# Kernel optimization log

Hardware: AMD Instinct MI355X
Metric: run time of the kernel (lower is better)

Reference implementation:

```python
import jax, jax.numpy as jnp
import numpy as np

NEG_INF = -1e30

def _rotate_half(x):
    x1, x2 = jnp.split(x, 2, axis=-1)
    return jnp.concatenate([-x2, x1], axis=-1)

def _apply_rope(x, sin, cos):
    # x: [b, t, h, d]; sin/cos: [t, d]
    s = sin[None, :, None, :]
    c = cos[None, :, None, :]
    return x * c + _rotate_half(x) * s

def setup_inputs() -> dict:
    key = jax.random.key(0)
    ks = jax.random.split(key, 5)
    B, T, D, H = 2, 2048, 2048, 16
    hd = D // H
    x = jax.random.normal(ks[0], (B, T, D), dtype=jnp.float32)
    sin = jax.random.normal(ks[1], (T, hd), dtype=jnp.float32)
    cos = jax.random.normal(ks[2], (T, hd), dtype=jnp.float32)
    W_qkv = jax.random.normal(ks[3], (D, D + 2 * hd), dtype=jnp.float32) * (1.0 / np.sqrt(D))
    W_o = jax.random.normal(ks[4], (D, D), dtype=jnp.float32) * (1.0 / np.sqrt(D))
    return {"x": x, "sin": sin, "cos": cos, "W_qkv": W_qkv, "W_o": W_o}

def reference(x, sin, cos, W_qkv, W_o):
    B, T, D = x.shape
    num_heads = 16
    head_dim = D // num_heads
    scale = head_dim ** (-0.5)

    qkv = x @ W_qkv                              # [B, T, D + 2*hd]
    q, k, v = jnp.split(qkv, [D, D + head_dim], axis=-1)
    # q -> [B, H, T, hd]; k, v single KV head -> [B, 1, T, hd]
    q = q.reshape(B, T, num_heads, head_dim).transpose(0, 2, 1, 3)
    k = k[:, :, None, :].transpose(0, 2, 1, 3)   # [B, 1, T, hd]
    v = v[:, :, None, :].transpose(0, 2, 1, 3)

    # module scales q by head_dim^-0.5 BEFORE rope/attention
    q = q * scale

    # apply_rope_safe: transpose to [B, T, H, hd], apply rope, transpose back
    q = _apply_rope(q.transpose(0, 2, 1, 3), sin, cos).transpose(0, 2, 1, 3)
    k = _apply_rope(k.transpose(0, 2, 1, 3), sin, cos).transpose(0, 2, 1, 3)

    k0 = k[:, 0]                                 # [B, T, hd] (MQA shared KV)
    v0 = v[:, 0]

    # jax.nn.dot_product_attention applies its own 1/sqrt(hd) scaling on top
    scores = jnp.einsum('bhqd,bkd->bhqk', q, k0) * scale
    causal = jnp.tril(jnp.ones((T, T), dtype=bool))
    scores = jnp.where(causal[None, None], scores, NEG_INF)
    probs = jax.nn.softmax(scores, axis=-1)
    out = jnp.einsum('bhqk,bkd->bhqd', probs, v0)  # [B, H, T, hd]

    out = out.transpose(0, 2, 1, 3).reshape(B, T, D)
    return out @ W_o
```

## Files before the change

### kernel.cpp

```cpp
#include <hip/hip_runtime.h>
#include <stdint.h>

typedef __bf16 bf16x8_t __attribute__((ext_vector_type(8)));
typedef float f32x4_t __attribute__((ext_vector_type(4)));

#define AS1 __attribute__((address_space(1)))
#define AS3 __attribute__((address_space(3)))

static __device__ __forceinline__ unsigned short f2bf(float f) {
  union { float f; unsigned u; } a;
  a.f = f;
  unsigned r = a.u + 0x7fffu + ((a.u >> 16) & 1u);
  return (unsigned short)(r >> 16);
}

static __device__ __forceinline__ unsigned pack2bf(float lo, float hi) {
  return (unsigned)f2bf(lo) | ((unsigned)f2bf(hi) << 16);
}

__global__ void cvt_bf16_kernel(const float* __restrict__ in, unsigned short* __restrict__ out) {
  long i = ((long)blockIdx.x * blockDim.x + threadIdx.x) * 4;
  float4 v = *(const float4*)(in + i);
  ushort4 o;
  o.x = f2bf(v.x);
  o.y = f2bf(v.y);
  o.z = f2bf(v.z);
  o.w = f2bf(v.w);
  *(ushort4*)(out + i) = o;
}

__global__ void transpose_f32_bf16(const float* __restrict__ src, unsigned short* __restrict__ dst,
                                   int ld, int dld, long sbs, long dbs) {
  __shared__ float tile[64][65];
  src += (long)blockIdx.z * sbs;
  dst += (long)blockIdx.z * dbs;
  const int c0 = blockIdx.x * 64, r0 = blockIdx.y * 64;
  const int tx = threadIdx.x, ty = threadIdx.y;
#pragma unroll
  for (int j = 0; j < 64; j += 4)
    tile[ty + j][tx] = src[(long)(r0 + ty + j) * ld + (c0 + tx)];
  __syncthreads();
#pragma unroll
  for (int j = 0; j < 64; j += 4)
    dst[(long)(c0 + ty + j) * dld + (r0 + tx)] = f2bf(tile[tx][ty + j]);
}

__global__ __launch_bounds__(256) void gemm_bt(const unsigned short* __restrict__ A,
                                               const unsigned short* __restrict__ Bt,
                                               float* __restrict__ C,
                                               int M, int N, int K) {
  __shared__ unsigned short As[128 * 32];
  __shared__ unsigned short Bs[128 * 32];
  const int tid = threadIdx.x;
  const int wid = tid >> 6, lane = tid & 63;
  const int r16 = lane & 15, g = lane >> 4;
  const long bm = (long)blockIdx.y * 128;
  const long bn = (long)blockIdx.x * 128;
  const int wr = (wid >> 1) * 64, wc = (wid & 1) * 64;
  f32x4_t acc[4][4];
#pragma unroll
  for (int i = 0; i < 4; i++)
#pragma unroll
    for (int j = 0; j < 4; j++) acc[i][j] = (f32x4_t){0.f, 0.f, 0.f, 0.f};

  for (int kt = 0; kt < K; kt += 32) {
#pragma unroll
    for (int i = 0; i < 2; i++) {
      const int chunk = (i * 4 + wid) * 64 + lane;
      const int row = chunk >> 2, col = (chunk & 3) * 8;
      __builtin_amdgcn_global_load_lds(
          (const AS1 void*)(A + (bm + row) * K + kt + col),
          (AS3 void*)(As + chunk * 8), 16, 0, 0);
      __builtin_amdgcn_global_load_lds(
          (const AS1 void*)(Bt + (bn + row) * K + kt + col),
          (AS3 void*)(Bs + chunk * 8), 16, 0, 0);
    }
    __syncthreads();
    bf16x8_t af[4], bfr[4];
#pragma unroll
    for (int mi = 0; mi < 4; mi++)
      af[mi] = *(const bf16x8_t*)(As + (wr + mi * 16 + r16) * 32 + g * 8);
#pragma unroll
    for (int ni = 0; ni < 4; ni++)
      bfr[ni] = *(const bf16x8_t*)(Bs + (wc + ni * 16 + r16) * 32 + g * 8);
#pragma unroll
    for (int mi = 0; mi < 4; mi++)
#pragma unroll
      for (int ni = 0; ni < 4; ni++)
        acc[mi][ni] = __builtin_amdgcn_mfma_f32_16x16x32_bf16(af[mi], bfr[ni], acc[mi][ni], 0, 0, 0);
    __syncthreads();
  }
#pragma unroll
  for (int mi = 0; mi < 4; mi++)
#pragma unroll
    for (int ni = 0; ni < 4; ni++) {
      const long rowb = bm + wr + mi * 16 + 4 * g;
      const long colb = bn + wc + ni * 16 + r16;
#pragma unroll
      for (int j = 0; j < 4; j++)
        C[(rowb + j) * N + colb] = acc[mi][ni][j];
    }
}

__global__ void rope_kernel(const float* __restrict__ qkv,
                            const float* __restrict__ sinp,
                            const float* __restrict__ cosp,
                            unsigned short* __restrict__ qr,
                            unsigned short* __restrict__ kr) {
  const int row = blockIdx.x;
  const int b = row >> 11, t = row & 2047;
  const float* src = qkv + (long)row * 2304;
  const int tid = threadIdx.x;
  const int d = tid & 127;
  const int dp = (d + 64) & 127;
  const float c = cosp[t * 128 + d];
  const float s = sinp[t * 128 + d];
  const float sgn = (d < 64) ? -1.f : 1.f;
  for (int h = (tid >> 7); h < 16; h += 2) {
    const float x0 = src[h * 128 + d];
    const float xp = src[h * 128 + dp];
    qr[((long)((b * 16 + h) * 2048 + t)) * 128 + d] = f2bf((x0 * c + sgn * xp * s) * 0.0078125f);
  }
  if (tid < 128) {
    const float x0 = src[2048 + d];
    const float xp = src[2048 + dp];
    kr[((long)(b * 2048 + t)) * 128 + d] = f2bf(x0 * c + sgn * xp * s);
  }
}

__global__ __launch_bounds__(256, 2)
void mqa_attn(const unsigned short* __restrict__ qr,
              const unsigned short* __restrict__ kr,
              const unsigned short* __restrict__ vT,
              unsigned short* __restrict__ ao) {
  __shared__ unsigned short Kb[2][64 * 128];
  __shared__ unsigned short Vb[128 * 64];
  __shared__ unsigned short plds[4][16 * 64];
  const int idx = blockIdx.x;
  const int pj = idx & 15, h = (idx >> 4) & 15, b = idx >> 8;
  const int tid = threadIdx.x;
  const int wid = tid >> 6, lane = tid & 63;
  const int r = lane & 15, g = lane >> 4;
  const int rs = r & 7;
  char* pw = (char*)&plds[wid][0];

  const unsigned short* kbase = kr + (long)b * 2048 * 128;
  const unsigned short* vbase = vT + (long)b * 128 * 2048;
  const unsigned short* qh = qr + (long)(b * 16 + h) * 2048 * 128;

  const int scol = (tid & 15) ^ ((tid >> 4) & 7);
  const int vscol = (tid & 7) ^ ((tid >> 3) & 7);

  f32x4_t o[8];
#pragma unroll
  for (int i = 0; i < 8; i++) o[i] = (f32x4_t){0.f, 0.f, 0.f, 0.f};
  float m = 0.f, lsum = 0.f;

  int tile = pj;
  bf16x8_t qf[4];
  {
    const unsigned short* qp = qh + (long)(tile * 64 + wid * 16 + r) * 128 + g * 8;
#pragma unroll
    for (int c = 0; c < 4; c++) qf[c] = *(const bf16x8_t*)(qp + c * 32);
  }

#pragma unroll
  for (int i = 0; i < 4; i++) {
    const int row = i * 16 + (tid >> 4);
    __builtin_amdgcn_global_load_lds(
        (const AS1 void*)(kbase + (long)row * 128 + scol * 8),
        (AS3 void*)(&Kb[0][(i * 256 + tid) * 8]), 16, 0, 0);
  }
  asm volatile("s_waitcnt vmcnt(0)" ::: "memory");
  __builtin_amdgcn_s_barrier();

  const int switch_s = pj + 1;
  for (int s = 0; s <= 32; s++) {
    const int cur = s & 1;
    const int kv0 = (s <= pj) ? 64 * s : 64 * (s - 1 - pj);

    if (s == switch_s) {
      float lt = lsum;
      lt += __shfl_xor(lt, 16);
      lt += __shfl_xor(lt, 32);
      float rl[4];
#pragma unroll
      for (int jj = 0; jj < 4; jj++) rl[jj] = 1.0f / __shfl(lt, 4 * g + jj);
      unsigned short* aop = ao + ((long)(b * 2048 + tile * 64 + wid * 16 + 4 * g)) * 2048 + h * 128 + r;
#pragma unroll
      for (int dt = 0; dt < 8; dt++)
#pragma unroll
        for (int jj = 0; jj < 4; jj++)
          aop[(long)jj * 2048 + dt * 16] = f2bf(o[dt][jj] * rl[jj]);
      tile = 31 - pj;
      const unsigned short* qp = qh + (long)(tile * 64 + wid * 16 + r) * 128 + g * 8;
#pragma unroll
      for (int c = 0; c < 4; c++) qf[c] = *(const bf16x8_t*)(qp + c * 32);
#pragma unroll
      for (int i = 0; i < 8; i++) o[i] = (f32x4_t){0.f, 0.f, 0.f, 0.f};
      m = 0.f;
      lsum = 0.f;
    }

#pragma unroll
    for (int i = 0; i < 4; i++) {
      const int vrow = i * 32 + (tid >> 3);
      __builtin_amdgcn_global_load_lds(
          (const AS1 void*)(vbase + (long)vrow * 2048 + kv0 + vscol * 8),
          (AS3 void*)(&Vb[(i * 256 + tid) * 8]), 16, 0, 0);
    }
    if (s < 32) {
      const int kvn = (s + 1 <= pj) ? 64 * (s + 1) : 64 * (s - pj);
#pragma unroll
      for (int i = 0; i < 4; i++) {
        const int row = i * 16 + (tid >> 4);
        __builtin_amdgcn_global_load_lds(
            (const AS1 void*)(kbase + (long)(kvn + row) * 128 + scol * 8),
            (AS3 void*)(&Kb[cur ^ 1][(i * 256 + tid) * 8]), 16, 0, 0);
      }
    }
    __builtin_amdgcn_sched_barrier(0);

    f32x4_t sc[4];
#pragma unroll
    for (int t = 0; t < 4; t++) sc[t] = (f32x4_t){0.f, 0.f, 0.f, 0.f};
    const unsigned short* Kcur = &Kb[cur][0];
    __builtin_amdgcn_s_setprio(1);
#pragma unroll
    for (int t = 0; t < 4; t++) {
      const unsigned short* krow = Kcur + (16 * t + r) * 128;
#pragma unroll
      for (int c = 0; c < 4; c++) {
        const bf16x8_t kf = *(const bf16x8_t*)(krow + (((4 * c + g) ^ rs) << 3));
        sc[t] = __builtin_amdgcn_mfma_f32_16x16x32_bf16(kf, qf[c], sc[t], 0, 0, 0);
      }
    }
    __builtin_amdgcn_s_setprio(0);

    if (s == pj || s == 32) {
#pragma unroll
      for (int t = 0; t < 4; t++)
#pragma unroll
        for (int jj = 0; jj < 4; jj++)
          if (t * 16 + 4 * g + jj > wid * 16 + r) sc[t][jj] = -1e30f;
    }
    float lm = sc[0][0];
#pragma unroll
    for (int t = 0; t < 4; t++)
#pragma unroll
      for (int jj = 0; jj < 4; jj++) lm = fmaxf(lm, sc[t][jj]);
    if (!__all(lm <= m + 8.f)) {
      float pm = lm;
      pm = fmaxf(pm, __shfl_xor(pm, 16));
      pm = fmaxf(pm, __shfl_xor(pm, 32));
      const float mnew = fmaxf(m, pm);
      const float alpha = __expf(m - mnew);
      lsum *= alpha;
      float aj[4];
#pragma unroll
      for (int jj = 0; jj < 4; jj++) aj[jj] = __shfl(alpha, 4 * g + jj);
#pragma unroll
      for (int dt = 0; dt < 8; dt++) {
        o[dt][0] *= aj[0]; o[dt][1] *= aj[1]; o[dt][2] *= aj[2]; o[dt][3] *= aj[3];
      }
      m = mnew;
    }
    float p[16];
#pragma unroll
    for (int t = 0; t < 4; t++)
#pragma unroll
      for (int jj = 0; jj < 4; jj++) p[4 * t + jj] = __expf(sc[t][jj] - m);
    float ls = 0.f;
#pragma unroll
    for (int i = 0; i < 16; i++) ls += p[i];
    lsum += ls;

    asm volatile("" ::: "memory");
#pragma unroll
    for (int t = 0; t < 4; t++) {
      uint2 w = {pack2bf(p[4 * t], p[4 * t + 1]), pack2bf(p[4 * t + 2], p[4 * t + 3])};
      *(uint2*)(pw + r * 128 + (((2 * t + (g >> 1)) ^ rs) << 4) + ((g & 1) << 3)) = w;
    }
    asm volatile("s_waitcnt lgkmcnt(0)" ::: "memory");
    const bf16x8_t pa0 = *(const bf16x8_t*)(pw + r * 128 + ((g ^ rs) << 4));
    const bf16x8_t pa1 = *(const bf16x8_t*)(pw + r * 128 + (((4 + g) ^ rs) << 4));

    if (s < 32)
      asm volatile("s_waitcnt vmcnt(4)" ::: "memory");
    else
      asm volatile("s_waitcnt vmcnt(0)" ::: "memory");
    __builtin_amdgcn_s_barrier();

    __builtin_amdgcn_s_setprio(1);
#pragma unroll
    for (int dt = 0; dt < 8; dt++) {
      const bf16x8_t vfA = *(const bf16x8_t*)(Vb + (dt * 16 + r) * 64 + ((g ^ rs) << 3));
      o[dt] = __builtin_amdgcn_mfma_f32_16x16x32_bf16(pa0, vfA, o[dt], 0, 0, 0);
    }
#pragma unroll
    for (int dt = 0; dt < 8; dt++) {
      const bf16x8_t vfB = *(const bf16x8_t*)(Vb + (dt * 16 + r) * 64 + (((4 + g) ^ rs) << 3));
      o[dt] = __builtin_amdgcn_mfma_f32_16x16x32_bf16(pa1, vfB, o[dt], 0, 0, 0);
    }
    __builtin_amdgcn_s_setprio(0);

    asm volatile("s_waitcnt vmcnt(0)" ::: "memory");
    __builtin_amdgcn_s_barrier();
  }
  {
    float lt = lsum;
    lt += __shfl_xor(lt, 16);
    lt += __shfl_xor(lt, 32);
    float rl[4];
#pragma unroll
    for (int jj = 0; jj < 4; jj++) rl[jj] = 1.0f / __shfl(lt, 4 * g + jj);
    unsigned short* aop = ao + ((long)(b * 2048 + tile * 64 + wid * 16 + 4 * g)) * 2048 + h * 128 + r;
#pragma unroll
    for (int dt = 0; dt < 8; dt++)
#pragma unroll
      for (int jj = 0; jj < 4; jj++)
        aop[(long)jj * 2048 + dt * 16] = f2bf(o[dt][jj] * rl[jj]);
  }
}

extern "C" void kernel_launch(void* const* d_in, const int* in_sizes, int n_in,
                              void* d_out, int out_size, void* d_ws, size_t ws_size,
                              hipStream_t stream) {
  const float* x    = (const float*)d_in[0];
  const float* sinp = (const float*)d_in[1];
  const float* cosp = (const float*)d_in[2];
  const float* Wqkv = (const float*)d_in[3];
  const float* Wo   = (const float*)d_in[4];
  float* out = (float*)d_out;
  char* ws = (char*)d_ws;

  const int B = 2, T = 2048, D = 2048, H = 16, HD = 128;
  const int M = B * T;
  const int NQ = D + 2 * HD;

  unsigned short* xb    = (unsigned short*)(ws + 0);
  unsigned short* wqkvT = (unsigned short*)(ws + 16777216);
  unsigned short* woT   = (unsigned short*)(ws + 26214400);
  float*          qkv   = (float*)         (ws + 34603008);
  unsigned short* qr    = (unsigned short*)(ws + 72351744);
  unsigned short* kr    = (unsigned short*)(ws + 89128960);
  unsigned short* vT    = (unsigned short*)(ws + 90177536);
  unsigned short* ao    = xb;

  dim3 tb(64, 4);
  cvt_bf16_kernel<<<(M * D) / 1024, 256, 0, stream>>>(x, xb);
  transpose_f32_bf16<<<dim3(NQ / 64, D / 64, 1), tb, 0, stream>>>(Wqkv, wqkvT, NQ, D, 0, 0);
  transpose_f32_bf16<<<dim3(D / 64, D / 64, 1), tb, 0, stream>>>(Wo, woT, D, D, 0, 0);
  gemm_bt<<<dim3(NQ / 128, M / 128), 256, 0, stream>>>(xb, wqkvT, qkv, M, NQ, D);
  rope_kernel<<<M, 256, 0, stream>>>(qkv, sinp, cosp, qr, kr);
  transpose_f32_bf16<<<dim3(HD / 64, T / 64, B), tb, 0, stream>>>(
      qkv + 2176, vT, NQ, T, (long)T * NQ, (long)HD * T);
  mqa_attn<<<dim3(512), 256, 0, stream>>>(qr, kr, vT, ao);
  gemm_bt<<<dim3(D / 128, M / 128), 256, 0, stream>>>(ao, woT, out, M, D, D);
}
```

Measured before the change: 223.3 us.

## Split-K both GEMMs in two with atomic accumulation and XCD-aware block swizzle

Both projection GEMMs now split the K dimension in half, launching twice as many workgroups that each accumulate partial results into zero-initialized outputs with float atomicAdd. A block-index swizzle maps consecutive blocks across the eight XCDs for better L2 locality. This targets low occupancy of the 128x128-tile grid (about 288 and 256 tiles on 256 CUs). It adds two zeroing kernels, atomic write traffic and extra memory passes over the fp32 outputs.

After: 296.5 us. 1.33x slower.

```diff
diff --git a/kernel.cpp b/kernel.cpp
--- a/kernel.cpp
+++ b/kernel.cpp
@@ -16,6 +16,11 @@
 
 static __device__ __forceinline__ unsigned pack2bf(float lo, float hi) {
   return (unsigned)f2bf(lo) | ((unsigned)f2bf(hi) << 16);
+}
+
+__global__ void zero_f32(float* __restrict__ p, long n4) {
+  long i = (long)blockIdx.x * blockDim.x + threadIdx.x;
+  if (i < n4) *(float4*)(p + i * 4) = make_float4(0.f, 0.f, 0.f, 0.f);
 }
 
 __global__ void cvt_bf16_kernel(const float* __restrict__ in, unsigned short* __restrict__ out) {
@@ -45,17 +50,28 @@
     dst[(long)(c0 + ty + j) * dld + (r0 + tx)] = f2bf(tile[tx][ty + j]);
 }
 
-__global__ __launch_bounds__(256) void gemm_bt(const unsigned short* __restrict__ A,
-                                               const unsigned short* __restrict__ Bt,
-                                               float* __restrict__ C,
-                                               int M, int N, int K) {
+__global__ __launch_bounds__(256) void gemm_bt_sk(const unsigned short* __restrict__ A,
+                                                  const unsigned short* __restrict__ Bt,
+                                                  float* __restrict__ C,
+                                                  int M, int N, int K, int nx, int ny) {
   __shared__ unsigned short As[128 * 32];
   __shared__ unsigned short Bs[128 * 32];
+  const int nwg = nx * ny * 2;
+  const int bid = blockIdx.x;
+  const int swz = (bid & 7) * (nwg >> 3) + (bid >> 3);
+  const int per = nx * ny;
+  const int bz = swz / per;
+  const int rem = swz - bz * per;
+  const int by = rem / nx;
+  const int bx = rem - by * nx;
+  const int Kh = K >> 1;
+  const int k0 = bz * Kh;
+
   const int tid = threadIdx.x;
   const int wid = tid >> 6, lane = tid & 63;
   const int r16 = lane & 15, g = lane >> 4;
-  const long bm = (long)blockIdx.y * 128;
-  const long bn = (long)blockIdx.x * 128;
+  const long bm = (long)by * 128;
+  const long bn = (long)bx * 128;
   const int wr = (wid >> 1) * 64, wc = (wid & 1) * 64;
   f32x4_t acc[4][4];
 #pragma unroll
@@ -63,7 +79,7 @@
 #pragma unroll
     for (int j = 0; j < 4; j++) acc[i][j] = (f32x4_t){0.f, 0.f, 0.f, 0.f};
 
-  for (int kt = 0; kt < K; kt += 32) {
+  for (int kt = k0; kt < k0 + Kh; kt += 32) {
 #pragma unroll
     for (int i = 0; i < 2; i++) {
       const int chunk = (i * 4 + wid) * 64 + lane;
@@ -98,7 +114,7 @@
       const long colb = bn + wc + ni * 16 + r16;
 #pragma unroll
       for (int j = 0; j < 4; j++)
-        C[(rowb + j) * N + colb] = acc[mi][ni][j];
+        atomicAdd(&C[(rowb + j) * N + colb], acc[mi][ni][j]);
     }
 }
 
@@ -347,14 +363,19 @@
   unsigned short* vT    = (unsigned short*)(ws + 90177536);
   unsigned short* ao    = xb;
 
+  const long nqkv = (long)M * NQ;
+  const long nout = (long)M * D;
+
   dim3 tb(64, 4);
+  zero_f32<<<(int)(nqkv / 4 + 255) / 256, 256, 0, stream>>>(qkv, nqkv / 4);
+  zero_f32<<<(int)(nout / 4 + 255) / 256, 256, 0, stream>>>(out, nout / 4);
   cvt_bf16_kernel<<<(M * D) / 1024, 256, 0, stream>>>(x, xb);
   transpose_f32_bf16<<<dim3(NQ / 64, D / 64, 1), tb, 0, stream>>>(Wqkv, wqkvT, NQ, D, 0, 0);
   transpose_f32_bf16<<<dim3(D / 64, D / 64, 1), tb, 0, stream>>>(Wo, woT, D, D, 0, 0);
-  gemm_bt<<<dim3(NQ / 128, M / 128), 256, 0, stream>>>(xb, wqkvT, qkv, M, NQ, D);
+  gemm_bt_sk<<<dim3((NQ / 128) * (M / 128) * 2), 256, 0, stream>>>(xb, wqkvT, qkv, M, NQ, D, NQ / 128, M / 128);
   rope_kernel<<<M, 256, 0, stream>>>(qkv, sinp, cosp, qr, kr);
   transpose_f32_bf16<<<dim3(HD / 64, T / 64, B), tb, 0, stream>>>(
       qkv + 2176, vT, NQ, T, (long)T * NQ, (long)HD * T);
   mqa_attn<<<dim3(512), 256, 0, stream>>>(qr, kr, vT, ao);
-  gemm_bt<<<dim3(D / 128, M / 128), 256, 0, stream>>>(ao, woT, out, M, D, D);
-}
+  gemm_bt_sk<<<dim3((D / 128) * (M / 128) * 2), 256, 0, stream>>>(ao, woT, out, M, D, D, D / 128, M / 128);
+}
```

## Triple-buffer GEMM LDS loads, swizzle LDS layout, and remap blocks for XCD locality

Applied to the files above, without the earlier changes.

The bf16 GEMM now keeps three LDS stages and issues global-to-LDS loads two k-tiles ahead, using vmcnt waits and a single barrier per iteration instead of two syncthreads. The LDS k-chunk slots are XOR-swizzled to reduce bank conflicts on the fragment reads. Raising wave priority around the MFMA block is also added. The grid is flattened and block ids are remapped so that consecutive tiles land on the same XCD for better L2 reuse. This triples the shared memory per block, which may lower occupancy.

After: 203.0 us. 9.1% less time.

```diff
diff --git a/kernel.cpp b/kernel.cpp
--- a/kernel.cpp
+++ b/kernel.cpp
@@ -48,48 +48,80 @@
 __global__ __launch_bounds__(256) void gemm_bt(const unsigned short* __restrict__ A,
                                                const unsigned short* __restrict__ Bt,
                                                float* __restrict__ C,
-                                               int M, int N, int K) {
-  __shared__ unsigned short As[128 * 32];
-  __shared__ unsigned short Bs[128 * 32];
+                                               int M, int N, int K, int nx) {
+  __shared__ unsigned short As[3][128 * 32];
+  __shared__ unsigned short Bs[3][128 * 32];
+  const int nwg = gridDim.x;
+  const int bid = blockIdx.x;
+  const int swz = (bid & 7) * (nwg >> 3) + (bid >> 3);
+  const int by = swz / nx;
+  const int bx = swz - by * nx;
+
   const int tid = threadIdx.x;
   const int wid = tid >> 6, lane = tid & 63;
   const int r16 = lane & 15, g = lane >> 4;
-  const long bm = (long)blockIdx.y * 128;
-  const long bn = (long)blockIdx.x * 128;
+  const long bm = (long)by * 128;
+  const long bn = (long)bx * 128;
   const int wr = (wid >> 1) * 64, wc = (wid & 1) * 64;
+  const int gr = g ^ (r16 & 3);
+  const int sslot = (lane & 3) ^ ((lane >> 2) & 3);
+
   f32x4_t acc[4][4];
 #pragma unroll
   for (int i = 0; i < 4; i++)
 #pragma unroll
     for (int j = 0; j < 4; j++) acc[i][j] = (f32x4_t){0.f, 0.f, 0.f, 0.f};
 
-  for (int kt = 0; kt < K; kt += 32) {
-#pragma unroll
-    for (int i = 0; i < 2; i++) {
-      const int chunk = (i * 4 + wid) * 64 + lane;
-      const int row = chunk >> 2, col = (chunk & 3) * 8;
-      __builtin_amdgcn_global_load_lds(
-          (const AS1 void*)(A + (bm + row) * K + kt + col),
-          (AS3 void*)(As + chunk * 8), 16, 0, 0);
-      __builtin_amdgcn_global_load_lds(
-          (const AS1 void*)(Bt + (bn + row) * K + kt + col),
-          (AS3 void*)(Bs + chunk * 8), 16, 0, 0);
-    }
-    __syncthreads();
+  const int NT = K >> 5;
+
+#define STAGE_G(buf, kt)                                                              \
+  {                                                                                   \
+    _Pragma("unroll") for (int i = 0; i < 2; i++) {                                   \
+      const int chunk = (i * 4 + wid) * 64 + lane;                                    \
+      const int row = chunk >> 2;                                                     \
+      __builtin_amdgcn_global_load_lds(                                               \
+          (const AS1 void*)(A + (bm + row) * K + (kt) + sslot * 8),                   \
+          (AS3 void*)(&As[buf][chunk * 8]), 16, 0, 0);                                \
+      __builtin_amdgcn_global_load_lds(                                               \
+          (const AS1 void*)(Bt + (bn + row) * K + (kt) + sslot * 8),                  \
+          (AS3 void*)(&Bs[buf][chunk * 8]), 16, 0, 0);                                \
+    }                                                                                 \
+  }
+
+  STAGE_G(0, 0)
+  STAGE_G(1, 32)
+  asm volatile("s_waitcnt vmcnt(4)" ::: "memory");
+  __builtin_amdgcn_s_barrier();
+
+  for (int T = 0; T < NT; T++) {
+    const int cur = T % 3;
+    if (T + 2 < NT) {
+      const int nb = (T + 2) % 3;
+      STAGE_G(nb, (T + 2) * 32)
+    }
+    __builtin_amdgcn_sched_barrier(0);
     bf16x8_t af[4], bfr[4];
 #pragma unroll
     for (int mi = 0; mi < 4; mi++)
-      af[mi] = *(const bf16x8_t*)(As + (wr + mi * 16 + r16) * 32 + g * 8);
+      af[mi] = *(const bf16x8_t*)(&As[cur][(wr + mi * 16 + r16) * 32 + gr * 8]);
 #pragma unroll
     for (int ni = 0; ni < 4; ni++)
-      bfr[ni] = *(const bf16x8_t*)(Bs + (wc + ni * 16 + r16) * 32 + g * 8);
+      bfr[ni] = *(const bf16x8_t*)(&Bs[cur][(wc + ni * 16 + r16) * 32 + gr * 8]);
+    __builtin_amdgcn_s_setprio(1);
 #pragma unroll
     for (int mi = 0; mi < 4; mi++)
 #pragma unroll
       for (int ni = 0; ni < 4; ni++)
         acc[mi][ni] = __builtin_amdgcn_mfma_f32_16x16x32_bf16(af[mi], bfr[ni], acc[mi][ni], 0, 0, 0);
-    __syncthreads();
-  }
+    __builtin_amdgcn_s_setprio(0);
+    if (T + 2 < NT)
+      asm volatile("s_waitcnt vmcnt(4)" ::: "memory");
+    else
+      asm volatile("s_waitcnt vmcnt(0)" ::: "memory");
+    __builtin_amdgcn_s_barrier();
+  }
+#undef STAGE_G
+
 #pragma unroll
   for (int mi = 0; mi < 4; mi++)
 #pragma unroll
@@ -351,10 +383,10 @@
   cvt_bf16_kernel<<<(M * D) / 1024, 256, 0, stream>>>(x, xb);
   transpose_f32_bf16<<<dim3(NQ / 64, D / 64, 1), tb, 0, stream>>>(Wqkv, wqkvT, NQ, D, 0, 0);
   transpose_f32_bf16<<<dim3(D / 64, D / 64, 1), tb, 0, stream>>>(Wo, woT, D, D, 0, 0);
-  gemm_bt<<<dim3(NQ / 128, M / 128), 256, 0, stream>>>(xb, wqkvT, qkv, M, NQ, D);
+  gemm_bt<<<dim3((NQ / 128) * (M / 128)), 256, 0, stream>>>(xb, wqkvT, qkv, M, NQ, D, NQ / 128);
   rope_kernel<<<M, 256, 0, stream>>>(qkv, sinp, cosp, qr, kr);
   transpose_f32_bf16<<<dim3(HD / 64, T / 64, B), tb, 0, stream>>>(
       qkv + 2176, vT, NQ, T, (long)T * NQ, (long)HD * T);
   mqa_attn<<<dim3(512), 256, 0, stream>>>(qr, kr, vT, ao);
-  gemm_bt<<<dim3(D / 128, M / 128), 256, 0, stream>>>(ao, woT, out, M, D, D);
-}
+  gemm_bt<<<dim3((D / 128) * (M / 128)), 256, 0, stream>>>(ao, woT, out, M, D, D, D / 128);
+}
```
